# Kernel tuning notes

Measured on AMD Instinct MI355X. Metric: run time of the kernel, lower is better.

## Reference

```python
import jax, jax.numpy as jnp
import numpy as np

B, L, D_MODEL = 2, 2048, 1024
D_INNER, D_STATE, D_CONV, DT_RANK = 2048, 16, 4, 64  # expand=2, dt_rank=ceil(1024/16)


def setup_inputs() -> dict:
    key = jax.random.key(0)
    ks = jax.random.split(key, 12)
    s = lambda k, shape, sc=0.02: jax.random.normal(k, shape, dtype=jnp.float32) * sc
    return {
        "x": jax.random.normal(ks[0], (B, L, D_MODEL), dtype=jnp.float32),
        "norm_w": jnp.ones((D_MODEL,), jnp.float32),
        "norm_b": jnp.zeros((D_MODEL,), jnp.float32),
        "in_proj_w": s(ks[1], (2 * D_INNER, D_MODEL)),
        "conv_w": s(ks[2], (D_INNER, 1, D_CONV), 0.1),
        "conv_b": s(ks[3], (D_INNER,), 0.1),
        "x_proj_w": s(ks[4], (DT_RANK + 2 * D_STATE, D_INNER)),
        "dt_proj_w": s(ks[5], (D_INNER, DT_RANK), 0.1),
        "dt_proj_b": s(ks[6], (D_INNER,), 0.5),
        "A_log": jnp.log(jnp.broadcast_to(jnp.arange(1, D_STATE + 1, dtype=jnp.float32), (D_INNER, D_STATE))),
        "D": jnp.ones((D_INNER,), jnp.float32),
        "out_proj_w": s(ks[7], (D_MODEL, D_INNER)),
    }


def _layernorm(x, w, b, eps=1e-5):
    mu = jnp.mean(x, axis=-1, keepdims=True)
    var = jnp.var(x, axis=-1, keepdims=True)
    return (x - mu) * jax.lax.rsqrt(var + eps) * w + b


def _mamba_forward(x, norm_w, norm_b, in_proj_w, conv_w, conv_b, x_proj_w,
                   dt_proj_w, dt_proj_b, A_log, D, out_proj_w):
    residual = x
    xn = _layernorm(x, norm_w, norm_b)
    # in_proj -> split into x-branch and gate z
    xz = jnp.einsum('bld,ed->ble', xn, in_proj_w)  # [B,L,2*D_INNER]
    xc, z = jnp.split(xz, 2, axis=-1)
    # causal depthwise conv1d over time
    xt = jnp.transpose(xc, (0, 2, 1))  # [B,C,L]
    xt = jnp.pad(xt, ((0, 0), (0, 0), (D_CONV - 1, 0)))
    xt = jax.lax.conv_general_dilated(
        xt, conv_w, window_strides=(1,), padding=[(0, 0)],
        feature_group_count=D_INNER,
        dimension_numbers=('NCH', 'OIH', 'NCH')) + conv_b[None, :, None]
    u = jax.nn.silu(jnp.transpose(xt, (0, 2, 1)))  # [B,L,D_INNER]
    # input-dependent dt, B, C
    x_dbl = jnp.einsum('bld,ed->ble', u, x_proj_w)
    dt, Bm, Cm = jnp.split(x_dbl, [DT_RANK, DT_RANK + D_STATE], axis=-1)
    dt = jax.nn.softplus(jnp.einsum('blr,dr->bld', dt, dt_proj_w) + dt_proj_b)  # [B,L,D_INNER]
    A = -jnp.exp(A_log)  # [D_INNER, D_STATE]

    def step(h, inp):
        dt_t, B_t, C_t, u_t = inp  # [B,Di],[B,Ds],[B,Ds],[B,Di]
        dA = jnp.exp(dt_t[..., None] * A)                       # [B,Di,Ds]
        h = dA * h + (dt_t * u_t)[..., None] * B_t[:, None, :]  # [B,Di,Ds]
        y_t = jnp.einsum('bds,bs->bd', h, C_t)
        return h, y_t

    xs = (jnp.transpose(dt, (1, 0, 2)), jnp.transpose(Bm, (1, 0, 2)),
          jnp.transpose(Cm, (1, 0, 2)), jnp.transpose(u, (1, 0, 2)))
    h0 = jnp.zeros((B, D_INNER, D_STATE), dtype=x.dtype)
    _, ys = jax.lax.scan(step, h0, xs)
    y = jnp.transpose(ys, (1, 0, 2)) + u * D  # [B,L,D_INNER]
    y = y * jax.nn.silu(z)
    out = jnp.einsum('ble,de->bld', y, out_proj_w)
    # dropout in eval mode = identity
    return residual + out


def reference(x, norm_w, norm_b, in_proj_w, conv_w, conv_b, x_proj_w,
              dt_proj_w, dt_proj_b, A_log, D, out_proj_w):
    return _mamba_forward(x, norm_w, norm_b, in_proj_w, conv_w, conv_b, x_proj_w,
                          dt_proj_w, dt_proj_b, A_log, D, out_proj_w)
```

## Files before the change

### kernel.cpp

```cpp
#include <hip/hip_runtime.h>
#include <hip/hip_bf16.h>
#include <math.h>

#define BB 2
#define LL 2048
#define DMODEL 1024
#define DINNER 2048
#define DSTATE 16
#define DTRANK 64
#define NROWS (BB * LL)
#define NC 64
#define CK 32
#define KS 16
#define KCH (DINNER / KS)

typedef __bf16 bf16x8 __attribute__((ext_vector_type(8)));
typedef float  f32x4  __attribute__((ext_vector_type(4)));
typedef ushort us8    __attribute__((ext_vector_type(8)));
typedef __attribute__((address_space(3))) void       as3_void;
typedef const __attribute__((address_space(1))) void as1_cvoid;

__device__ __forceinline__ ushort f2bf(float x) {
    __hip_bfloat16 h = __float2bfloat16(x);
    return *(ushort*)&h;
}
__device__ __forceinline__ float bf2f(ushort u) {
    unsigned int v = ((unsigned int)u) << 16;
    return *(float*)&v;
}

__global__ __launch_bounds__(256) void ln_kernel(const float* __restrict__ x,
                                                 const float* __restrict__ w,
                                                 const float* __restrict__ b,
                                                 __hip_bfloat16* __restrict__ xn) {
    int row = blockIdx.x;
    const float* xr = x + (size_t)row * DMODEL;
    float4 v = reinterpret_cast<const float4*>(xr)[threadIdx.x];
    float s  = v.x + v.y + v.z + v.w;
    float ss = v.x * v.x + v.y * v.y + v.z * v.z + v.w * v.w;
    for (int off = 32; off > 0; off >>= 1) {
        s  += __shfl_down(s, off);
        ss += __shfl_down(ss, off);
    }
    __shared__ float red0[4], red1[4];
    __shared__ float mu_s, rstd_s;
    int lane = threadIdx.x & 63, wv = threadIdx.x >> 6;
    if (lane == 0) { red0[wv] = s; red1[wv] = ss; }
    __syncthreads();
    if (threadIdx.x == 0) {
        float S = red0[0] + red0[1] + red0[2] + red0[3];
        float SS = red1[0] + red1[1] + red1[2] + red1[3];
        float mu = S * (1.0f / DMODEL);
        float var = SS * (1.0f / DMODEL) - mu * mu;
        mu_s = mu;
        rstd_s = rsqrtf(var + 1e-5f);
    }
    __syncthreads();
    float mu = mu_s, rstd = rstd_s;
    float4 wv4 = reinterpret_cast<const float4*>(w)[threadIdx.x];
    float4 bv4 = reinterpret_cast<const float4*>(b)[threadIdx.x];
    ushort4 o;
    o.x = f2bf((v.x - mu) * rstd * wv4.x + bv4.x);
    o.y = f2bf((v.y - mu) * rstd * wv4.y + bv4.y);
    o.z = f2bf((v.z - mu) * rstd * wv4.z + bv4.z);
    o.w = f2bf((v.w - mu) * rstd * wv4.w + bv4.w);
    *reinterpret_cast<ushort4*>((ushort*)xn + (size_t)row * DMODEL + threadIdx.x * 4) = o;
}

__global__ __launch_bounds__(256) void cvt_kernel(const float* __restrict__ in,
                                                  __hip_bfloat16* __restrict__ o) {
    int i = (blockIdx.x * 256 + threadIdx.x) * 4;
    float4 v = *reinterpret_cast<const float4*>(in + i);
    ushort4 p;
    p.x = f2bf(v.x); p.y = f2bf(v.y); p.z = f2bf(v.z); p.w = f2bf(v.w);
    *reinterpret_cast<ushort4*>((ushort*)o + i) = p;
}

template <int EPI>
__global__ __launch_bounds__(256) void gemm_bf16(
    const __hip_bfloat16* __restrict__ A, int lda,
    const __hip_bfloat16* __restrict__ W, int ldw,
    void* __restrict__ C, void* __restrict__ C2, int nsplit, int ldc,
    int K, const float* __restrict__ R) {
    __shared__ ushort As[128][32];
    __shared__ ushort Bs[128][32];
    int tid = threadIdx.x;
    int w = tid >> 6, lane = tid & 63;
    int nx = gridDim.x;
    int id = blockIdx.y * nx + blockIdx.x;
    int q = (nx * gridDim.y) >> 3;
    int swz = (id & 7) * q + (id >> 3);
    int bx = swz % nx, by = swz / nx;
    int m0 = by * 128, n0 = bx * 128;
    int wr = w >> 1, wc = w & 1;

    int srow = (w << 4) + (lane >> 2);
    int skoff = (lane & 3) << 3;
    const ushort* gA = (const ushort*)A + (size_t)(m0 + srow) * lda + skoff;
    const ushort* gB = (const ushort*)W + (size_t)(n0 + srow) * ldw + skoff;
    char* ldsA0 = (char*)&As[0][0] + w * 1024;
    char* ldsB0 = (char*)&Bs[0][0] + w * 1024;

    f32x4 acc[4][4] = {};
    int frow = (lane & 15);
    int fk   = (lane >> 4) << 3;

    for (int k0 = 0; k0 < K; k0 += 32) {
        __syncthreads();
        __builtin_amdgcn_global_load_lds((as1_cvoid*)(gA + k0),                    (as3_void*)(ldsA0),        16, 0, 0);
        __builtin_amdgcn_global_load_lds((as1_cvoid*)(gA + (size_t)64 * lda + k0), (as3_void*)(ldsA0 + 4096), 16, 0, 0);
        __builtin_amdgcn_global_load_lds((as1_cvoid*)(gB + k0),                    (as3_void*)(ldsB0),        16, 0, 0);
        __builtin_amdgcn_global_load_lds((as1_cvoid*)(gB + (size_t)64 * ldw + k0), (as3_void*)(ldsB0 + 4096), 16, 0, 0);
        __syncthreads();

        bf16x8 af[4], bfr[4];
#pragma unroll
        for (int mi = 0; mi < 4; mi++)
            af[mi] = *(const bf16x8*)&As[wr * 64 + mi * 16 + frow][fk];
#pragma unroll
        for (int ni = 0; ni < 4; ni++)
            bfr[ni] = *(const bf16x8*)&Bs[wc * 64 + ni * 16 + frow][fk];
#pragma unroll
        for (int mi = 0; mi < 4; mi++)
#pragma unroll
            for (int ni = 0; ni < 4; ni++)
                acc[mi][ni] = __builtin_amdgcn_mfma_f32_16x16x32_bf16(
                    af[mi], bfr[ni], acc[mi][ni], 0, 0, 0);
    }

    int crow = (lane >> 4) << 2;
    int ccol = lane & 15;
    bool toz = (EPI == 0) && (n0 >= nsplit);
    int nbase = toz ? (n0 - nsplit) : n0;
    ushort* Cu = toz ? (ushort*)C2 : (ushort*)C;
#pragma unroll
    for (int mi = 0; mi < 4; mi++) {
#pragma unroll
        for (int ni = 0; ni < 4; ni++) {
#pragma unroll
            for (int r = 0; r < 4; r++) {
                int m = m0 + wr * 64 + mi * 16 + crow + r;
                int n = nbase + wc * 64 + ni * 16 + ccol;
                float v = acc[mi][ni][r];
                if (EPI == 2) {
                    v += R[(size_t)m * ldc + n];
                    ((float*)C)[(size_t)m * ldc + n] = v;
                } else {
                    Cu[(size_t)m * ldc + n] = f2bf(v);
                }
            }
        }
    }
}

template <int EPI>
__global__ __launch_bounds__(256) void gemm_kernel(
    const float* __restrict__ A, int lda,
    const float* __restrict__ W, int ldw,
    float* __restrict__ C, int ldc,
    int N, int K,
    const float* __restrict__ bias) {
    __shared__ float As[16][64];
    __shared__ float Ws[16][64];
    int m0 = blockIdx.y * 64;
    int n0 = blockIdx.x * 64;
    int tid = threadIdx.x;
    int tm = tid >> 4, tn = tid & 15;
    int lr = tid >> 2;
    int lk = (tid & 3) << 2;

    float acc[4][4] = {};

    for (int k0 = 0; k0 < K; k0 += 16) {
        float4 av = *reinterpret_cast<const float4*>(A + (size_t)(m0 + lr) * lda + k0 + lk);
        float4 wvv;
        int wn = n0 + lr;
        if (wn < N)
            wvv = *reinterpret_cast<const float4*>(W + (size_t)wn * ldw + k0 + lk);
        else
            wvv = make_float4(0.f, 0.f, 0.f, 0.f);
        __syncthreads();
        As[lk + 0][lr] = av.x; As[lk + 1][lr] = av.y;
        As[lk + 2][lr] = av.z; As[lk + 3][lr] = av.w;
        Ws[lk + 0][lr] = wvv.x; Ws[lk + 1][lr] = wvv.y;
        Ws[lk + 2][lr] = wvv.z; Ws[lk + 3][lr] = wvv.w;
        __syncthreads();
#pragma unroll
        for (int k = 0; k < 16; k++) {
            float4 a = *reinterpret_cast<const float4*>(&As[k][tm << 2]);
            float4 bv = *reinterpret_cast<const float4*>(&Ws[k][tn << 2]);
            float ar[4] = {a.x, a.y, a.z, a.w};
            float br[4] = {bv.x, bv.y, bv.z, bv.w};
#pragma unroll
            for (int i = 0; i < 4; i++)
#pragma unroll
                for (int j = 0; j < 4; j++)
                    acc[i][j] = fmaf(ar[i], br[j], acc[i][j]);
        }
    }
#pragma unroll
    for (int i = 0; i < 4; i++) {
        int m = m0 + (tm << 2) + i;
#pragma unroll
        for (int j = 0; j < 4; j++) {
            int n = n0 + (tn << 2) + j;
            if (n < N) {
                float v = acc[i][j];
                if (EPI == 1) {
                    v += bias[n];
                    v = (v > 20.f) ? v : log1pf(__expf(v));
                    ((ushort*)C)[(size_t)m * ldc + n] = f2bf(v);
                } else {
                    C[(size_t)m * ldc + n] = v;
                }
            }
        }
    }
}

__global__ __launch_bounds__(256) void xp_partial(
    const ushort* __restrict__ A,
    const float* __restrict__ W,
    float* __restrict__ P) {
    __shared__ float As[16][64];
    __shared__ float Ws[16][64];
    int m0 = blockIdx.y * 64;
    int n0 = blockIdx.x * 64;
    int kbase = blockIdx.z * KCH;
    int tid = threadIdx.x;
    int tm = tid >> 4, tn = tid & 15;
    int lr = tid >> 2;
    int lk = (tid & 3) << 2;

    float acc[4][4] = {};

    for (int k0 = kbase; k0 < kbase + KCH; k0 += 16) {
        ushort4 au = *reinterpret_cast<const ushort4*>(A + (size_t)(m0 + lr) * DINNER + k0 + lk);
        float4 av = make_float4(bf2f(au.x), bf2f(au.y), bf2f(au.z), bf2f(au.w));
        float4 wvv;
        int wn = n0 + lr;
        if (wn < 96)
            wvv = *reinterpret_cast<const float4*>(W + (size_t)wn * DINNER + k0 + lk);
        else
            wvv = make_float4(0.f, 0.f, 0.f, 0.f);
        __syncthreads();
        As[lk + 0][lr] = av.x; As[lk + 1][lr] = av.y;
        As[lk + 2][lr] = av.z; As[lk + 3][lr] = av.w;
        Ws[lk + 0][lr] = wvv.x; Ws[lk + 1][lr] = wvv.y;
        Ws[lk + 2][lr] = wvv.z; Ws[lk + 3][lr] = wvv.w;
        __syncthreads();
#pragma unroll
        for (int k = 0; k < 16; k++) {
            float4 a = *reinterpret_cast<const float4*>(&As[k][tm << 2]);
            float4 bv = *reinterpret_cast<const float4*>(&Ws[k][tn << 2]);
            float ar[4] = {a.x, a.y, a.z, a.w};
            float br[4] = {bv.x, bv.y, bv.z, bv.w};
#pragma unroll
            for (int i = 0; i < 4; i++)
#pragma unroll
                for (int j = 0; j < 4; j++)
                    acc[i][j] = fmaf(ar[i], br[j], acc[i][j]);
        }
    }
    float* Pz = P + (size_t)blockIdx.z * NROWS * 96;
#pragma unroll
    for (int i = 0; i < 4; i++) {
        int m = m0 + (tm << 2) + i;
#pragma unroll
        for (int j = 0; j < 4; j++) {
            int n = n0 + (tn << 2) + j;
            if (n < 96)
                Pz[(size_t)m * 96 + n] = acc[i][j];
        }
    }
}

__global__ __launch_bounds__(256) void xp_reduce(
    const float* __restrict__ P, float* __restrict__ xdbl) {
    int i = blockIdx.x * 256 + threadIdx.x;
    float s = 0.f;
#pragma unroll
    for (int z = 0; z < KS; z++)
        s += P[(size_t)z * NROWS * 96 + i];
    xdbl[i] = s;
}

__global__ __launch_bounds__(256) void conv_silu_kernel(
    const ushort* __restrict__ xc16, const float* __restrict__ cw,
    const float* __restrict__ cb, ushort* __restrict__ u16) {
    int r = blockIdx.x;
    int l = r & (LL - 1);
    int c0 = threadIdx.x << 3;
    const ushort* base = xc16 + (size_t)r * DINNER + c0;
    us8 z8 = {0, 0, 0, 0, 0, 0, 0, 0};
    us8 v0 = *(const us8*)(base);
    us8 v1 = (l >= 1) ? *(const us8*)(base - DINNER)     : z8;
    us8 v2 = (l >= 2) ? *(const us8*)(base - 2 * DINNER) : z8;
    us8 v3 = (l >= 3) ? *(const us8*)(base - 3 * DINNER) : z8;
    us8 o;
#pragma unroll
    for (int j = 0; j < 8; j++) {
        float4 wj = reinterpret_cast<const float4*>(cw)[c0 + j];
        float acc = cb[c0 + j];
        acc = fmaf(bf2f(v3[j]), wj.x, acc);
        acc = fmaf(bf2f(v2[j]), wj.y, acc);
        acc = fmaf(bf2f(v1[j]), wj.z, acc);
        acc = fmaf(bf2f(v0[j]), wj.w, acc);
        float sig = 1.f / (1.f + __expf(-acc));
        o[j] = f2bf(acc * sig);
    }
    *(us8*)(u16 + (size_t)r * DINNER + c0) = o;
}

__global__ __launch_bounds__(256) void scan_pass1(
    const ushort* __restrict__ dt16, const ushort* __restrict__ u16,
    const float* __restrict__ xdbl, const float* __restrict__ A_log,
    float* __restrict__ hloc, float* __restrict__ aprod) {
    int bc = blockIdx.x >> 3;
    int b = bc >> 6, c = bc & (NC - 1);
    int d = ((blockIdx.x & 7) << 8) + threadIdx.x;
    float a2[DSTATE];
#pragma unroll
    for (int s = 0; s < DSTATE; s++)
        a2[s] = -__expf(A_log[d * DSTATE + s]) * 1.44269504089f;
    float h[DSTATE], ap[DSTATE];
#pragma unroll
    for (int s = 0; s < DSTATE; s++) { h[s] = 0.f; ap[s] = 1.f; }

    int t0 = c * CK;
    const ushort* dtp = dt16 + ((size_t)b * LL + t0) * DINNER + d;
    const ushort* up  = u16  + ((size_t)b * LL + t0) * DINNER + d;
    const float* xr0  = xdbl + ((size_t)b * LL + t0) * 96;

    for (int t = 0; t < CK; t++) {
        float dtv = bf2f(dtp[(size_t)t * DINNER]);
        float uv  = bf2f(up[(size_t)t * DINNER]);
        float du  = dtv * uv;
        const float* xr = xr0 + t * 96;
#pragma unroll
        for (int s = 0; s < DSTATE; s++) {
            float dA = exp2f(dtv * a2[s]);
            h[s] = fmaf(dA, h[s], du * xr[64 + s]);
            ap[s] *= dA;
        }
    }
    size_t base = ((size_t)bc * DSTATE) * DINNER + d;
#pragma unroll
    for (int s = 0; s < DSTATE; s++) {
        hloc[base + (size_t)s * DINNER]  = h[s];
        aprod[base + (size_t)s * DINNER] = ap[s];
    }
}

__global__ __launch_bounds__(256) void scan_pass2(
    float* __restrict__ hloc, const float* __restrict__ aprod) {
    int idx = blockIdx.x * 256 + threadIdx.x;
    int d = idx & (DINNER - 1);
    int s = (idx >> 11) & (DSTATE - 1);
    int b = idx >> 15;
    float run = 0.f;
    for (int c = 0; c < NC; c++) {
        size_t off = ((size_t)((b * NC + c) * DSTATE + s)) * DINNER + d;
        float hl = hloc[off];
        float ap = aprod[off];
        hloc[off] = run;
        run = fmaf(ap, run, hl);
    }
}

__global__ __launch_bounds__(256) void scan_pass3(
    const ushort* __restrict__ dt16, const ushort* __restrict__ u16,
    const float* __restrict__ xdbl, const ushort* __restrict__ zb,
    const float* __restrict__ A_log, const float* __restrict__ Dp,
    const float* __restrict__ hinit, __hip_bfloat16* __restrict__ y) {
    int bc = blockIdx.x >> 3;
    int b = bc >> 6, c = bc & (NC - 1);
    int d = ((blockIdx.x & 7) << 8) + threadIdx.x;
    float a2[DSTATE];
#pragma unroll
    for (int s = 0; s < DSTATE; s++)
        a2[s] = -__expf(A_log[d * DSTATE + s]) * 1.44269504089f;
    float Dd = Dp[d];
    float h[DSTATE];
    size_t base = ((size_t)bc * DSTATE) * DINNER + d;
#pragma unroll
    for (int s = 0; s < DSTATE; s++) h[s] = hinit[base + (size_t)s * DINNER];

    int t0 = c * CK;
    const ushort* dtp = dt16 + ((size_t)b * LL + t0) * DINNER + d;
    const ushort* up  = u16  + ((size_t)b * LL + t0) * DINNER + d;
    const ushort* zp  = zb   + ((size_t)b * LL + t0) * DINNER + d;
    const float* xr0  = xdbl + ((size_t)b * LL + t0) * 96;
    ushort* yp = (ushort*)y + ((size_t)b * LL + t0) * DINNER + d;

    for (int t = 0; t < CK; t++) {
        float dtv = bf2f(dtp[(size_t)t * DINNER]);
        float uv  = bf2f(up[(size_t)t * DINNER]);
        float du  = dtv * uv;
        const float* xr = xr0 + t * 96;
        float yv = 0.f;
#pragma unroll
        for (int s = 0; s < DSTATE; s++) {
            float dA = exp2f(dtv * a2[s]);
            h[s] = fmaf(dA, h[s], du * xr[64 + s]);
            yv = fmaf(h[s], xr[80 + s], yv);
        }
        float zv = bf2f(zp[(size_t)t * DINNER]);
        float sig = 1.f / (1.f + __expf(-zv));
        yv = (yv + uv * Dd) * (zv * sig);
        yp[(size_t)t * DINNER] = f2bf(yv);
    }
}

extern "C" void kernel_launch(void* const* d_in, const int* in_sizes, int n_in,
                              void* d_out, int out_size, void* d_ws, size_t ws_size,
                              hipStream_t stream) {
    const float* x         = (const float*)d_in[0];
    const float* norm_w    = (const float*)d_in[1];
    const float* norm_b    = (const float*)d_in[2];
    const float* in_proj_w = (const float*)d_in[3];
    const float* conv_w    = (const float*)d_in[4];
    const float* conv_b    = (const float*)d_in[5];
    const float* x_proj_w  = (const float*)d_in[6];
    const float* dt_proj_w = (const float*)d_in[7];
    const float* dt_proj_b = (const float*)d_in[8];
    const float* A_log     = (const float*)d_in[9];
    const float* Dp        = (const float*)d_in[10];
    const float* out_proj_w= (const float*)d_in[11];
    float* out = (float*)d_out;

    float* ws   = (float*)d_ws;
    const size_t NI = (size_t)NROWS * DINNER;
    ushort* xc16 = (ushort*)ws;
    ushort* zb   = (ushort*)(ws + NI / 2);
    ushort* u16  = (ushort*)(ws + NI);
    ushort* dt16 = (ushort*)(ws + NI + NI / 2);
    float*  xdbl = ws + 2 * NI;
    __hip_bfloat16* xnb = (__hip_bfloat16*)(xdbl + (size_t)NROWS * 96);
    __hip_bfloat16* ybb = xnb + (size_t)NROWS * DMODEL;
    __hip_bfloat16* wib = ybb + NI;
    __hip_bfloat16* wob = wib + (size_t)2 * DINNER * DMODEL;
    float* hloc  = (float*)(wob + (size_t)DMODEL * DINNER);
    float* aprod = hloc + NI / 2;
    float* xpp   = aprod + NI / 2;

    ln_kernel<<<NROWS, 256, 0, stream>>>(x, norm_w, norm_b, xnb);
    cvt_kernel<<<(2 * DINNER * DMODEL) / 1024, 256, 0, stream>>>(in_proj_w, wib);
    cvt_kernel<<<(DMODEL * DINNER) / 1024, 256, 0, stream>>>(out_proj_w, wob);
    gemm_bf16<0><<<dim3((2 * DINNER) / 128, NROWS / 128), 256, 0, stream>>>(
        xnb, DMODEL, wib, DMODEL, xc16, zb, DINNER, DINNER, DMODEL, nullptr);
    conv_silu_kernel<<<NROWS, 256, 0, stream>>>(xc16, conv_w, conv_b, u16);
    xp_partial<<<dim3(2, NROWS / 64, KS), 256, 0, stream>>>(u16, x_proj_w, xpp);
    xp_reduce<<<(NROWS * 96) / 256, 256, 0, stream>>>(xpp, xdbl);
    gemm_kernel<1><<<dim3(DINNER / 64, NROWS / 64), 256, 0, stream>>>(
        xdbl, 96, dt_proj_w, DTRANK, (float*)dt16, DINNER, DINNER, DTRANK, dt_proj_b);
    scan_pass1<<<BB * NC * (DINNER / 256), 256, 0, stream>>>(
        dt16, u16, xdbl, A_log, hloc, aprod);
    scan_pass2<<<(BB * DSTATE * DINNER) / 256, 256, 0, stream>>>(hloc, aprod);
    scan_pass3<<<BB * NC * (DINNER / 256), 256, 0, stream>>>(
        dt16, u16, xdbl, zb, A_log, Dp, hloc, ybb);
    gemm_bf16<2><<<dim3(DMODEL / 128, NROWS / 128), 256, 0, stream>>>(
        ybb, DINNER, wob, DINNER, out, nullptr, 1 << 30, DMODEL, DINNER, x);
}
```

Before: 420.4 us.

## Parallelize scan over state dim, move dt_proj to bf16 MFMA GEMM

The selective-scan kernels now map one thread per (channel, state) pair instead of one thread per channel looping over 16 states, and pass3 reduces the C-weighted sum with a 16-lane xor shuffle. The hloc/aprod layout becomes state-innermost so pass2 and the scan passes read it contiguously. The fp32 dt_proj GEMM is replaced by the bf16 MFMA GEMM, using a bf16 copy of x_dbl and converted dt_proj weights, with softplus fused into the epilogue. The block-index swizzle in the bf16 GEMM is removed. The changes risk redundant dt/u loads across 16 threads and extra precision loss in dt.

```diff
diff --git a/kernel.cpp b/kernel.cpp
--- a/kernel.cpp
+++ b/kernel.cpp
@@ -86,12 +86,7 @@
     __shared__ ushort Bs[128][32];
     int tid = threadIdx.x;
     int w = tid >> 6, lane = tid & 63;
-    int nx = gridDim.x;
-    int id = blockIdx.y * nx + blockIdx.x;
-    int q = (nx * gridDim.y) >> 3;
-    int swz = (id & 7) * q + (id >> 3);
-    int bx = swz % nx, by = swz / nx;
-    int m0 = by * 128, n0 = bx * 128;
+    int m0 = blockIdx.y * 128, n0 = blockIdx.x * 128;
     int wr = w >> 1, wc = w & 1;
 
     int srow = (w << 4) + (lane >> 2);
@@ -145,73 +140,12 @@
                 if (EPI == 2) {
                     v += R[(size_t)m * ldc + n];
                     ((float*)C)[(size_t)m * ldc + n] = v;
-                } else {
-                    Cu[(size_t)m * ldc + n] = f2bf(v);
-                }
-            }
-        }
-    }
-}
-
-template <int EPI>
-__global__ __launch_bounds__(256) void gemm_kernel(
-    const float* __restrict__ A, int lda,
-    const float* __restrict__ W, int ldw,
-    float* __restrict__ C, int ldc,
-    int N, int K,
-    const float* __restrict__ bias) {
-    __shared__ float As[16][64];
-    __shared__ float Ws[16][64];
-    int m0 = blockIdx.y * 64;
-    int n0 = blockIdx.x * 64;
-    int tid = threadIdx.x;
-    int tm = tid >> 4, tn = tid & 15;
-    int lr = tid >> 2;
-    int lk = (tid & 3) << 2;
-
-    float acc[4][4] = {};
-
-    for (int k0 = 0; k0 < K; k0 += 16) {
-        float4 av = *reinterpret_cast<const float4*>(A + (size_t)(m0 + lr) * lda + k0 + lk);
-        float4 wvv;
-        int wn = n0 + lr;
-        if (wn < N)
-            wvv = *reinterpret_cast<const float4*>(W + (size_t)wn * ldw + k0 + lk);
-        else
-            wvv = make_float4(0.f, 0.f, 0.f, 0.f);
-        __syncthreads();
-        As[lk + 0][lr] = av.x; As[lk + 1][lr] = av.y;
-        As[lk + 2][lr] = av.z; As[lk + 3][lr] = av.w;
-        Ws[lk + 0][lr] = wvv.x; Ws[lk + 1][lr] = wvv.y;
-        Ws[lk + 2][lr] = wvv.z; Ws[lk + 3][lr] = wvv.w;
-        __syncthreads();
-#pragma unroll
-        for (int k = 0; k < 16; k++) {
-            float4 a = *reinterpret_cast<const float4*>(&As[k][tm << 2]);
-            float4 bv = *reinterpret_cast<const float4*>(&Ws[k][tn << 2]);
-            float ar[4] = {a.x, a.y, a.z, a.w};
-            float br[4] = {bv.x, bv.y, bv.z, bv.w};
-#pragma unroll
-            for (int i = 0; i < 4; i++)
-#pragma unroll
-                for (int j = 0; j < 4; j++)
-                    acc[i][j] = fmaf(ar[i], br[j], acc[i][j]);
-        }
-    }
-#pragma unroll
-    for (int i = 0; i < 4; i++) {
-        int m = m0 + (tm << 2) + i;
-#pragma unroll
-        for (int j = 0; j < 4; j++) {
-            int n = n0 + (tn << 2) + j;
-            if (n < N) {
-                float v = acc[i][j];
-                if (EPI == 1) {
-                    v += bias[n];
+                } else if (EPI == 1) {
+                    v += R[n];
                     v = (v > 20.f) ? v : log1pf(__expf(v));
                     ((ushort*)C)[(size_t)m * ldc + n] = f2bf(v);
                 } else {
-                    C[(size_t)m * ldc + n] = v;
+                    Cu[(size_t)m * ldc + n] = f2bf(v);
                 }
             }
         }
@@ -276,13 +210,15 @@
 }
 
 __global__ __launch_bounds__(256) void xp_reduce(
-    const float* __restrict__ P, float* __restrict__ xdbl) {
+    const float* __restrict__ P, float* __restrict__ xdbl,
+    ushort* __restrict__ xdbl16) {
     int i = blockIdx.x * 256 + threadIdx.x;
     float s = 0.f;
 #pragma unroll
     for (int z = 0; z < KS; z++)
         s += P[(size_t)z * NROWS * 96 + i];
     xdbl[i] = s;
+    xdbl16[i] = f2bf(s);
 }
 
 __global__ __launch_bounds__(256) void conv_silu_kernel(
@@ -316,51 +252,44 @@
     const ushort* __restrict__ dt16, const ushort* __restrict__ u16,
     const float* __restrict__ xdbl, const float* __restrict__ A_log,
     float* __restrict__ hloc, float* __restrict__ aprod) {
-    int bc = blockIdx.x >> 3;
+    int gb = blockIdx.x;
+    int bc = gb >> 7;
     int b = bc >> 6, c = bc & (NC - 1);
-    int d = ((blockIdx.x & 7) << 8) + threadIdx.x;
-    float a2[DSTATE];
-#pragma unroll
-    for (int s = 0; s < DSTATE; s++)
-        a2[s] = -__expf(A_log[d * DSTATE + s]) * 1.44269504089f;
-    float h[DSTATE], ap[DSTATE];
-#pragma unroll
-    for (int s = 0; s < DSTATE; s++) { h[s] = 0.f; ap[s] = 1.f; }
+    int dg = gb & 127;
+    int tid = threadIdx.x;
+    int dl = tid >> 4, s = tid & 15;
+    int d = (dg << 4) + dl;
+
+    float a2 = -__expf(A_log[(dg << 8) + tid]) * 1.44269504089f;
+    float h = 0.f, ap = 1.f;
 
     int t0 = c * CK;
     const ushort* dtp = dt16 + ((size_t)b * LL + t0) * DINNER + d;
     const ushort* up  = u16  + ((size_t)b * LL + t0) * DINNER + d;
-    const float* xr0  = xdbl + ((size_t)b * LL + t0) * 96;
+    const float* xr0  = xdbl + ((size_t)b * LL + t0) * 96 + 64 + s;
 
     for (int t = 0; t < CK; t++) {
         float dtv = bf2f(dtp[(size_t)t * DINNER]);
         float uv  = bf2f(up[(size_t)t * DINNER]);
-        float du  = dtv * uv;
-        const float* xr = xr0 + t * 96;
-#pragma unroll
-        for (int s = 0; s < DSTATE; s++) {
-            float dA = exp2f(dtv * a2[s]);
-            h[s] = fmaf(dA, h[s], du * xr[64 + s]);
-            ap[s] *= dA;
-        }
-    }
-    size_t base = ((size_t)bc * DSTATE) * DINNER + d;
-#pragma unroll
-    for (int s = 0; s < DSTATE; s++) {
-        hloc[base + (size_t)s * DINNER]  = h[s];
-        aprod[base + (size_t)s * DINNER] = ap[s];
-    }
+        float Bv  = xr0[t * 96];
+        float dA  = exp2f(dtv * a2);
+        h  = fmaf(dA, h, dtv * uv * Bv);
+        ap *= dA;
+    }
+    size_t off = (((size_t)bc * DINNER + d) << 4) + s;
+    hloc[off]  = h;
+    aprod[off] = ap;
 }
 
 __global__ __launch_bounds__(256) void scan_pass2(
     float* __restrict__ hloc, const float* __restrict__ aprod) {
     int idx = blockIdx.x * 256 + threadIdx.x;
-    int d = idx & (DINNER - 1);
-    int s = (idx >> 11) & (DSTATE - 1);
+    int s = idx & 15;
+    int d = (idx >> 4) & (DINNER - 1);
     int b = idx >> 15;
     float run = 0.f;
     for (int c = 0; c < NC; c++) {
-        size_t off = ((size_t)((b * NC + c) * DSTATE + s)) * DINNER + d;
+        size_t off = ((((size_t)(b * NC + c)) * DINNER + d) << 4) + s;
         float hl = hloc[off];
         float ap = aprod[off];
         hloc[off] = run;
@@ -373,42 +302,42 @@
     const float* __restrict__ xdbl, const ushort* __restrict__ zb,
     const float* __restrict__ A_log, const float* __restrict__ Dp,
     const float* __restrict__ hinit, __hip_bfloat16* __restrict__ y) {
-    int bc = blockIdx.x >> 3;
+    int gb = blockIdx.x;
+    int bc = gb >> 7;
     int b = bc >> 6, c = bc & (NC - 1);
-    int d = ((blockIdx.x & 7) << 8) + threadIdx.x;
-    float a2[DSTATE];
-#pragma unroll
-    for (int s = 0; s < DSTATE; s++)
-        a2[s] = -__expf(A_log[d * DSTATE + s]) * 1.44269504089f;
+    int dg = gb & 127;
+    int tid = threadIdx.x;
+    int dl = tid >> 4, s = tid & 15;
+    int d = (dg << 4) + dl;
+
+    float a2 = -__expf(A_log[(dg << 8) + tid]) * 1.44269504089f;
     float Dd = Dp[d];
-    float h[DSTATE];
-    size_t base = ((size_t)bc * DSTATE) * DINNER + d;
-#pragma unroll
-    for (int s = 0; s < DSTATE; s++) h[s] = hinit[base + (size_t)s * DINNER];
+    float h = hinit[(((size_t)bc * DINNER + d) << 4) + s];
 
     int t0 = c * CK;
     const ushort* dtp = dt16 + ((size_t)b * LL + t0) * DINNER + d;
     const ushort* up  = u16  + ((size_t)b * LL + t0) * DINNER + d;
     const ushort* zp  = zb   + ((size_t)b * LL + t0) * DINNER + d;
-    const float* xr0  = xdbl + ((size_t)b * LL + t0) * 96;
+    const float* xr0  = xdbl + ((size_t)b * LL + t0) * 96 + 64 + s;
     ushort* yp = (ushort*)y + ((size_t)b * LL + t0) * DINNER + d;
 
     for (int t = 0; t < CK; t++) {
         float dtv = bf2f(dtp[(size_t)t * DINNER]);
         float uv  = bf2f(up[(size_t)t * DINNER]);
-        float du  = dtv * uv;
-        const float* xr = xr0 + t * 96;
-        float yv = 0.f;
-#pragma unroll
-        for (int s = 0; s < DSTATE; s++) {
-            float dA = exp2f(dtv * a2[s]);
-            h[s] = fmaf(dA, h[s], du * xr[64 + s]);
-            yv = fmaf(h[s], xr[80 + s], yv);
-        }
+        float Bv  = xr0[t * 96];
+        float Cv  = xr0[t * 96 + 16];
+        float dA  = exp2f(dtv * a2);
+        h = fmaf(dA, h, dtv * uv * Bv);
+        float p = h * Cv;
+        p += __shfl_xor(p, 1);
+        p += __shfl_xor(p, 2);
+        p += __shfl_xor(p, 4);
+        p += __shfl_xor(p, 8);
         float zv = bf2f(zp[(size_t)t * DINNER]);
         float sig = 1.f / (1.f + __expf(-zv));
-        yv = (yv + uv * Dd) * (zv * sig);
-        yp[(size_t)t * DINNER] = f2bf(yv);
+        float yv = (p + uv * Dd) * (zv * sig);
+        if (s == 0)
+            yp[(size_t)t * DINNER] = f2bf(yv);
     }
 }
 
@@ -431,33 +360,38 @@
 
     float* ws   = (float*)d_ws;
     const size_t NI = (size_t)NROWS * DINNER;
-    ushort* xc16 = (ushort*)ws;
-    ushort* zb   = (ushort*)(ws + NI / 2);
-    ushort* u16  = (ushort*)(ws + NI);
-    ushort* dt16 = (ushort*)(ws + NI + NI / 2);
-    float*  xdbl = ws + 2 * NI;
-    __hip_bfloat16* xnb = (__hip_bfloat16*)(xdbl + (size_t)NROWS * 96);
+    ushort* xc16  = (ushort*)ws;
+    ushort* zb    = (ushort*)(ws + NI / 2);
+    ushort* u16   = (ushort*)(ws + NI);
+    ushort* dt16  = (ushort*)(ws + NI + NI / 2);
+    float*  xdbl  = ws + 2 * NI;
+    ushort* xdbl16 = (ushort*)(xdbl + (size_t)NROWS * 96);
+    float*  nxt   = xdbl + (size_t)NROWS * 96 + (size_t)NROWS * 96 / 2;
+    __hip_bfloat16* xnb = (__hip_bfloat16*)nxt;
     __hip_bfloat16* ybb = xnb + (size_t)NROWS * DMODEL;
     __hip_bfloat16* wib = ybb + NI;
     __hip_bfloat16* wob = wib + (size_t)2 * DINNER * DMODEL;
-    float* hloc  = (float*)(wob + (size_t)DMODEL * DINNER);
+    __hip_bfloat16* wdt = wob + (size_t)DMODEL * DINNER;
+    float* hloc  = (float*)(wdt + (size_t)DINNER * DTRANK);
     float* aprod = hloc + NI / 2;
     float* xpp   = aprod + NI / 2;
 
     ln_kernel<<<NROWS, 256, 0, stream>>>(x, norm_w, norm_b, xnb);
     cvt_kernel<<<(2 * DINNER * DMODEL) / 1024, 256, 0, stream>>>(in_proj_w, wib);
     cvt_kernel<<<(DMODEL * DINNER) / 1024, 256, 0, stream>>>(out_proj_w, wob);
+    cvt_kernel<<<(DINNER * DTRANK) / 1024, 256, 0, stream>>>(dt_proj_w, wdt);
     gemm_bf16<0><<<dim3((2 * DINNER) / 128, NROWS / 128), 256, 0, stream>>>(
         xnb, DMODEL, wib, DMODEL, xc16, zb, DINNER, DINNER, DMODEL, nullptr);
     conv_silu_kernel<<<NROWS, 256, 0, stream>>>(xc16, conv_w, conv_b, u16);
     xp_partial<<<dim3(2, NROWS / 64, KS), 256, 0, stream>>>(u16, x_proj_w, xpp);
-    xp_reduce<<<(NROWS * 96) / 256, 256, 0, stream>>>(xpp, xdbl);
-    gemm_kernel<1><<<dim3(DINNER / 64, NROWS / 64), 256, 0, stream>>>(
-        xdbl, 96, dt_proj_w, DTRANK, (float*)dt16, DINNER, DINNER, DTRANK, dt_proj_b);
-    scan_pass1<<<BB * NC * (DINNER / 256), 256, 0, stream>>>(
+    xp_reduce<<<(NROWS * 96) / 256, 256, 0, stream>>>(xpp, xdbl, xdbl16);
+    gemm_bf16<1><<<dim3(DINNER / 128, NROWS / 128), 256, 0, stream>>>(
+        (const __hip_bfloat16*)xdbl16, 96, wdt, DTRANK,
+        dt16, nullptr, 1 << 30, DINNER, DTRANK, dt_proj_b);
+    scan_pass1<<<BB * NC * (DINNER / 16), 256, 0, stream>>>(
         dt16, u16, xdbl, A_log, hloc, aprod);
-    scan_pass2<<<(BB * DSTATE * DINNER) / 256, 256, 0, stream>>>(hloc, aprod);
-    scan_pass3<<<BB * NC * (DINNER / 256), 256, 0, stream>>>(
+    scan_pass2<<<(BB * DINNER * DSTATE) / 256, 256, 0, stream>>>(hloc, aprod);
+    scan_pass3<<<BB * NC * (DINNER / 16), 256, 0, stream>>>(
         dt16, u16, xdbl, zb, A_log, Dp, hloc, ybb);
     gemm_bf16<2><<<dim3(DMODEL / 128, NROWS / 128), 256, 0, stream>>>(
         ybb, DINNER, wob, DINNER, out, nullptr, 1 << 30, DMODEL, DINNER, x);
```

New measurement: 589.7 us. 40.3% more time.
